# Kernel tuning notes

Measured on AMD Instinct MI355X. Metric: run time of the kernel, lower is better.

Reference implementation:

```python
import jax, jax.numpy as jnp
import numpy as np

HEADS = 12
D_MODEL = 768
D_K = D_MODEL // HEADS
BS, SEQ = 2, 4096


def setup_inputs() -> dict:
    key = jax.random.key(0)
    ks = jax.random.split(key, 12)
    s = 1.0 / np.sqrt(D_MODEL)
    return {
        "q": jax.random.normal(ks[0], (BS, SEQ, D_MODEL), jnp.float32),
        "k": jax.random.normal(ks[1], (BS, SEQ, D_MODEL), jnp.float32),
        "v": jax.random.normal(ks[2], (BS, SEQ, D_MODEL), jnp.float32),
        "Wq": jax.random.normal(ks[3], (D_MODEL, D_MODEL), jnp.float32) * s,
        "bq": jax.random.normal(ks[4], (D_MODEL,), jnp.float32) * s,
        "Wk": jax.random.normal(ks[5], (D_MODEL, D_MODEL), jnp.float32) * s,
        "bk": jax.random.normal(ks[6], (D_MODEL,), jnp.float32) * s,
        "Wv": jax.random.normal(ks[7], (D_MODEL, D_MODEL), jnp.float32) * s,
        "bv": jax.random.normal(ks[8], (D_MODEL,), jnp.float32) * s,
        "Wo": jax.random.normal(ks[9], (D_MODEL, D_MODEL), jnp.float32) * s,
        "bo": jax.random.normal(ks[10], (D_MODEL,), jnp.float32) * s,
        "mask": jnp.ones((BS, 1, SEQ), jnp.int32),
    }


def reference(q, k, v, Wq, bq, Wk, bk, Wv, bv, Wo, bo, mask):
    bs, sq, _ = q.shape
    # torch Linear: x @ W.T + b; then reshape to (bs, S, h, d_k) and transpose to (bs, h, S, d_k)
    def proj(x, W, b):
        y = x @ W.T + b
        return y.reshape(bs, -1, HEADS, D_K).transpose(0, 2, 1, 3)
    qh, kh, vh = proj(q, Wq, bq), proj(k, Wk, bk), proj(v, Wv, bv)
    scores = jnp.einsum("bhqd,bhkd->bhqk", qh, kh) / np.sqrt(D_K)
    # mask.unsqueeze(1): [bs,1,1,S_kv], masked_fill where mask == 0
    scores = jnp.where(mask[:, None, :, :] == 0, jnp.float32(-1e9), scores)
    attn = jax.nn.softmax(scores, axis=-1)  # dropout = identity (eval mode)
    ctx = jnp.einsum("bhqk,bhkd->bhqd", attn, vh)
    concat = ctx.transpose(0, 2, 1, 3).reshape(bs, sq, D_MODEL)
    return concat @ Wo.T + bo
```

## Files before the change

kernel.cpp:

```cpp
#include <hip/hip_runtime.h>
#include <hip/hip_bf16.h>

typedef __bf16 bf16x8 __attribute__((ext_vector_type(8)));
typedef __bf16 bf16x4 __attribute__((ext_vector_type(4)));
typedef short s16x4 __attribute__((ext_vector_type(4)));
typedef float f32x4 __attribute__((ext_vector_type(4)));
typedef unsigned short u16;

#define HEADS 12
#define DK 64
#define DM 768
#define SEQL 4096
#define BSZ 2
#define MROWS (BSZ * SEQL)
#define WELEM (DM * DM)
#define NX 6291456
#define WTOT (4 * WELEM)
#define BTOT (4 * 768)

#define QSCALE 0.180336880434245f
#define EXP2F(x) __builtin_amdgcn_exp2f(x)

__device__ __forceinline__ float bf2f(u16 x) {
    unsigned int u = ((unsigned int)x) << 16;
    return __uint_as_float(u);
}
__device__ __forceinline__ u16 f2bf(float f) {
    unsigned int u = __float_as_uint(f);
    u += 0x7fff + ((u >> 16) & 1);
    return (u16)(u >> 16);
}
__device__ __forceinline__ unsigned int cvt_pk(float lo, float hi) {
#if __has_builtin(__builtin_amdgcn_cvt_pk_bf16_f32)
    auto r = __builtin_amdgcn_cvt_pk_bf16_f32(lo, hi);
    unsigned int u;
    __builtin_memcpy(&u, &r, 4);
    return u;
#else
    return (unsigned int)f2bf(lo) | ((unsigned int)f2bf(hi) << 16);
#endif
}

__device__ __forceinline__ f32x4 mfma16(bf16x4 a, bf16x4 b, f32x4 c) {
#if __has_builtin(__builtin_amdgcn_mfma_f32_16x16x16_bf16)
    return __builtin_amdgcn_mfma_f32_16x16x16_bf16(a, b, c, 0, 0, 0);
#elif __has_builtin(__builtin_amdgcn_mfma_f32_16x16x16bf16_1k)
    s16x4 ai, bi;
    __builtin_memcpy(&ai, &a, 8);
    __builtin_memcpy(&bi, &b, 8);
    return __builtin_amdgcn_mfma_f32_16x16x16bf16_1k(ai, bi, c, 0, 0, 0);
#else
    f32x4 d = c;
    asm("v_mfma_f32_16x16x16_bf16 %0, %1, %2, %0" : "+v"(d) : "v"(a), "v"(b));
    return d;
#endif
}

__global__ void detect_dtype(const u16* __restrict__ q, int* __restrict__ flag) {
    __shared__ int cnt;
    if (threadIdx.x == 0) cnt = 0;
    __syncthreads();
    int c = 0;
    for (int i = threadIdx.x; i < 16384; i += 256) {
        u16 x = q[i];
        if (((x >> 7) & 0xFF) == 0xFF) c++;
    }
    if (c) atomicAdd(&cnt, c);
    __syncthreads();
    if (threadIdx.x == 0) *flag = (cnt > 0) ? 1 : 0;
}

__global__ __launch_bounds__(256) void convert_x(
    const void* __restrict__ X0, const void* __restrict__ X1, const void* __restrict__ X2,
    u16* __restrict__ Xc, const int* __restrict__ flag) {
    const int f32m = *flag;
    int i8 = blockIdx.x * 256 + threadIdx.x;
    if (i8 >= 3 * NX / 8) return;
    int w = i8 / (NX / 8);
    int off8 = i8 - w * (NX / 8);
    const void* src = (w == 0) ? X0 : (w == 1) ? X1 : X2;
    u16* dst = Xc + (size_t)w * NX + (size_t)off8 * 8;
    if (f32m) {
        float4 f0 = ((const float4*)src)[off8 * 2];
        float4 f1 = ((const float4*)src)[off8 * 2 + 1];
        uint4 p = {cvt_pk(f0.x, f0.y), cvt_pk(f0.z, f0.w),
                   cvt_pk(f1.x, f1.y), cvt_pk(f1.z, f1.w)};
        *(uint4*)dst = p;
    } else {
        *(uint4*)dst = ((const uint4*)src)[off8];
    }
}

__global__ __launch_bounds__(256) void convert_wb(
    const void* __restrict__ W0, const void* __restrict__ W1,
    const void* __restrict__ W2, const void* __restrict__ W3,
    const void* __restrict__ B0, const void* __restrict__ B1,
    const void* __restrict__ B2, const void* __restrict__ B3,
    u16* __restrict__ Wc, u16* __restrict__ bc, const int* __restrict__ flag) {
    const int f32m = *flag;
    int i4 = blockIdx.x * 256 + threadIdx.x;
    const int n4 = (WTOT + BTOT) / 4;
    if (i4 >= n4) return;
    int base = i4 * 4;
    const void* src;
    u16* dst;
    int off;
    if (base < WTOT) {
        int w = base / WELEM;
        off = base - w * WELEM;
        src = (w == 0) ? W0 : (w == 1) ? W1 : (w == 2) ? W2 : W3;
        dst = Wc + w * WELEM + off;
    } else {
        int bi = base - WTOT;
        int w = bi / 768;
        off = bi - w * 768;
        src = (w == 0) ? B0 : (w == 1) ? B1 : (w == 2) ? B2 : B3;
        dst = bc + w * 768 + off;
    }
    if (f32m) {
        float4 f = *(const float4*)((const float*)src + off);
        uint2 p = {cvt_pk(f.x, f.y), cvt_pk(f.z, f.w)};
        *(uint2*)dst = p;
    } else {
        *(uint2*)dst = *(const uint2*)((const u16*)src + off);
    }
}

typedef __attribute__((address_space(1))) unsigned int glb_u32;
typedef __attribute__((address_space(3))) unsigned int lds_u32;

__device__ __forceinline__ void gld16(const u16* g, u16* l) {
    __builtin_amdgcn_global_load_lds((glb_u32*)g, (lds_u32*)l, 16, 0, 0);
}

template <int NCH>
__device__ __forceinline__ void stage_g(const u16* gbase, u16* lbase, int tid) {
#pragma unroll
    for (int it = 0; it < NCH / 256; ++it) {
        int c = it * 256 + tid;
        int row = c >> 2, p = c & 3;
        int gc = p ^ (row & 3);
        gld16(gbase + (size_t)row * DM + gc * 8, lbase + c * 8);
    }
}

__global__ __launch_bounds__(256) void gemm_qkv3(
    const u16* __restrict__ Xc, const u16* __restrict__ Wc, const u16* __restrict__ bc,
    u16* __restrict__ Yq, u16* __restrict__ Yk, u16* __restrict__ Yv) {
    __shared__ __align__(16) u16 As[2][128 * 32];
    __shared__ __align__(16) u16 Bs[2][128 * 32];

    const int by  = blockIdx.y;
    const int sel = by / 6;
    const int n0  = (by - sel * 6) * 128;
    const int m0  = blockIdx.x * 128;

    const u16* X  = Xc + (size_t)sel * NX;
    const u16* W  = Wc + (size_t)sel * WELEM;
    const u16* Bp = bc + sel * 768;
    u16* Y = sel == 0 ? Yq : (sel == 1 ? Yk : Yv);
    const float oscale = sel == 0 ? QSCALE : 1.0f;

    const int tid = threadIdx.x, lane = tid & 63, wave = tid >> 6;
    const int wr = (wave >> 1) * 64, wc2 = (wave & 1) * 64;
    const int l15 = lane & 15, quad = lane >> 4;
    const int ck = (quad ^ (l15 & 3)) * 8;

    f32x4 acc[4][4] = {};

    stage_g<512>(X + (size_t)m0 * DM, &As[0][0], tid);
    stage_g<512>(W + (size_t)n0 * DM, &Bs[0][0], tid);
    __syncthreads();

    for (int it = 0; it < 24; ++it) {
        const int cur = it & 1, nxt = cur ^ 1;
        if (it < 23) {
            stage_g<512>(X + (size_t)m0 * DM + (it + 1) * 32, &As[nxt][0], tid);
            stage_g<512>(W + (size_t)n0 * DM + (it + 1) * 32, &Bs[nxt][0], tid);
        }
        bf16x8 a[4], b[4];
#pragma unroll
        for (int i = 0; i < 4; ++i)
            a[i] = *(const bf16x8*)&As[cur][(wr + i * 16 + l15) * 32 + ck];
#pragma unroll
        for (int j = 0; j < 4; ++j)
            b[j] = *(const bf16x8*)&Bs[cur][(wc2 + j * 16 + l15) * 32 + ck];
#pragma unroll
        for (int i = 0; i < 4; ++i)
#pragma unroll
            for (int j = 0; j < 4; ++j)
                acc[i][j] = __builtin_amdgcn_mfma_f32_16x16x32_bf16(a[i], b[j], acc[i][j], 0, 0, 0);
        __syncthreads();
    }

#pragma unroll
    for (int j = 0; j < 4; ++j) {
        int o = n0 + wc2 + j * 16 + l15;
        float bv = bf2f(Bp[o]);
        int h = o >> 6, d = o & 63;
#pragma unroll
        for (int i = 0; i < 4; ++i) {
            int row0 = m0 + wr + i * 16 + quad * 4;
            int bb = row0 >> 12, s0 = row0 & (SEQL - 1);
            if (sel < 2) {
#pragma unroll
                for (int r = 0; r < 4; ++r)
                    Y[((bb * HEADS + h) << 18) + ((s0 + r) << 6) + d] =
                        f2bf((acc[i][j][r] + bv) * oscale);
            } else {
                uint2 p = {cvt_pk(acc[i][j][0] + bv, acc[i][j][1] + bv),
                           cvt_pk(acc[i][j][2] + bv, acc[i][j][3] + bv)};
                *(uint2*)&Y[((bb * HEADS + h) << 18) + (d << 12) + s0] = p;
            }
        }
    }
}

__global__ __launch_bounds__(256) void gemm_out3(const u16* __restrict__ X,
                                                 const u16* __restrict__ W,
                                                 const u16* __restrict__ Bp,
                                                 void* __restrict__ Y,
                                                 const int* __restrict__ flag) {
    __shared__ __align__(16) u16 As[2][64 * 32];
    __shared__ __align__(16) u16 Bs[2][128 * 32];

    const int f32mode = *flag;
    const int m0 = blockIdx.x * 64, n0 = blockIdx.y * 128;
    const int tid = threadIdx.x, lane = tid & 63, wave = tid >> 6;
    const int wr = (wave >> 1) * 32, wc2 = (wave & 1) * 64;
    const int l15 = lane & 15, quad = lane >> 4;
    const int ck = (quad ^ (l15 & 3)) * 8;

    f32x4 acc[2][4] = {};

    stage_g<256>(X + (size_t)m0 * DM, &As[0][0], tid);
    stage_g<512>(W + (size_t)n0 * DM, &Bs[0][0], tid);
    __syncthreads();

    for (int it = 0; it < 24; ++it) {
        const int cur = it & 1, nxt = cur ^ 1;
        if (it < 23) {
            stage_g<256>(X + (size_t)m0 * DM + (it + 1) * 32, &As[nxt][0], tid);
            stage_g<512>(W + (size_t)n0 * DM + (it + 1) * 32, &Bs[nxt][0], tid);
        }
        bf16x8 a[2], b[4];
#pragma unroll
        for (int i = 0; i < 2; ++i)
            a[i] = *(const bf16x8*)&As[cur][(wr + i * 16 + l15) * 32 + ck];
#pragma unroll
        for (int j = 0; j < 4; ++j)
            b[j] = *(const bf16x8*)&Bs[cur][(wc2 + j * 16 + l15) * 32 + ck];
#pragma unroll
        for (int i = 0; i < 2; ++i)
#pragma unroll
            for (int j = 0; j < 4; ++j)
                acc[i][j] = __builtin_amdgcn_mfma_f32_16x16x32_bf16(a[i], b[j], acc[i][j], 0, 0, 0);
        __syncthreads();
    }

#pragma unroll
    for (int j = 0; j < 4; ++j) {
        int o = n0 + wc2 + j * 16 + l15;
        float bv = bf2f(Bp[o]);
#pragma unroll
        for (int i = 0; i < 2; ++i)
#pragma unroll
            for (int r = 0; r < 4; ++r) {
                int row = m0 + wr + i * 16 + quad * 4 + r;
                float val = acc[i][j][r] + bv;
                if (f32mode) ((float*)Y)[(size_t)row * DM + o] = val;
                else         ((u16*)Y)[(size_t)row * DM + o] = f2bf(val);
            }
    }
}

__device__ __forceinline__ void stage8_bf16(u16* dst, const u16* src) {
    *(uint4*)dst = *(const uint4*)src;
}
__device__ __forceinline__ void stage16_bf16(u16* dst, const u16* src) {
    *(uint4*)dst = *(const uint4*)src;
    *(uint4*)(dst + 8) = *(const uint4*)(src + 8);
}
__device__ __forceinline__ void stage16_f32pk(u16* dst, const float* src) {
    float4 f0 = ((const float4*)src)[0];
    float4 f1 = ((const float4*)src)[1];
    float4 f2 = ((const float4*)src)[2];
    float4 f3 = ((const float4*)src)[3];
    uint4 lo = {cvt_pk(f0.x, f0.y), cvt_pk(f0.z, f0.w), cvt_pk(f1.x, f1.y), cvt_pk(f1.z, f1.w)};
    uint4 hi = {cvt_pk(f2.x, f2.y), cvt_pk(f2.z, f2.w), cvt_pk(f3.x, f3.y), cvt_pk(f3.z, f3.w)};
    *(uint4*)dst = lo;
    *(uint4*)(dst + 8) = hi;
}

__global__ __launch_bounds__(256) void gemm_qkv_fb(
    const void* __restrict__ Xq, const void* __restrict__ Xk, const void* __restrict__ Xv,
    const u16* __restrict__ Wc, const u16* __restrict__ bc,
    u16* __restrict__ Yq, u16* __restrict__ Yk, u16* __restrict__ Yv,
    const int* __restrict__ flag) {
    __shared__ __align__(16) u16 As[128][40];
    __shared__ __align__(16) u16 Bs[64][40];
    const int f32mode = *flag;
    const int by = blockIdx.y;
    const int sel = by / 12;
    const int n0 = (by - sel * 12) * 64;
    const int m0 = blockIdx.x * 128;
    const void* Xp = sel == 0 ? Xq : (sel == 1 ? Xk : Xv);
    const u16* Wp = Wc + sel * WELEM;
    const u16* Bp = bc + sel * 768;
    u16* Y = sel == 0 ? Yq : (sel == 1 ? Yk : Yv);
    const float oscale = sel == 0 ? QSCALE : 1.0f;
    const int tid = threadIdx.x, lane = tid & 63, wave = tid >> 6;
    const int wr = (wave >> 1) * 64, wc = (wave & 1) * 32;
    const int l15 = lane & 15, quad = lane >> 4;
    const int srA = tid >> 1, scA = (tid & 1) * 16;
    const int srB = tid >> 2, scB = (tid & 3) * 8;
    f32x4 acc[4][2] = {};
    const size_t xoff = (size_t)(m0 + srA) * DM + scA;
    const size_t woff = (size_t)(n0 + srB) * DM + scB;
    for (int kb = 0; kb < DM; kb += 32) {
        if (f32mode) stage16_f32pk(&As[srA][scA], (const float*)Xp + xoff + kb);
        else         stage16_bf16(&As[srA][scA], (const u16*)Xp + xoff + kb);
        stage8_bf16(&Bs[srB][scB], Wp + woff + kb);
        __syncthreads();
        bf16x8 a[4], b[2];
#pragma unroll
        for (int i = 0; i < 4; ++i) a[i] = *(const bf16x8*)&As[wr + i * 16 + l15][quad * 8];
#pragma unroll
        for (int j = 0; j < 2; ++j) b[j] = *(const bf16x8*)&Bs[wc + j * 16 + l15][quad * 8];
#pragma unroll
        for (int i = 0; i < 4; ++i)
#pragma unroll
            for (int j = 0; j < 2; ++j)
                acc[i][j] = __builtin_amdgcn_mfma_f32_16x16x32_bf16(a[i], b[j], acc[i][j], 0, 0, 0);
        __syncthreads();
    }
#pragma unroll
    for (int j = 0; j < 2; ++j) {
        int o = n0 + wc + j * 16 + l15;
        float bv = bf2f(Bp[o]);
#pragma unroll
        for (int i = 0; i < 4; ++i)
#pragma unroll
            for (int r = 0; r < 4; ++r) {
                int row = m0 + wr + i * 16 + quad * 4 + r;
                float val = (acc[i][j][r] + bv) * oscale;
                int bb = row >> 12, s = row & (SEQL - 1);
                int h = o >> 6, d = o & 63;
                if (sel < 2) Y[((bb * HEADS + h) << 18) + (s << 6) + d] = f2bf(val);
                else         Y[((bb * HEADS + h) << 18) + (d << 12) + s] = f2bf(val);
            }
    }
}

__global__ __launch_bounds__(256) void gemm_out_fb(const u16* __restrict__ X,
                                                   const u16* __restrict__ Wp,
                                                   const u16* __restrict__ Bp,
                                                   void* __restrict__ Y,
                                                   const int* __restrict__ flag) {
    __shared__ __align__(16) u16 As[128][40];
    __shared__ __align__(16) u16 Bs[64][40];
    const int f32mode = *flag;
    const int m0 = blockIdx.x * 128, n0 = blockIdx.y * 64;
    const int tid = threadIdx.x, lane = tid & 63, wave = tid >> 6;
    const int wr = (wave >> 1) * 64, wc = (wave & 1) * 32;
    const int l15 = lane & 15, quad = lane >> 4;
    const int srA = tid >> 1, scA = (tid & 1) * 16;
    const int srB = tid >> 2, scB = (tid & 3) * 8;
    f32x4 acc[4][2] = {};
    const size_t xoff = (size_t)(m0 + srA) * DM + scA;
    const size_t woff = (size_t)(n0 + srB) * DM + scB;
    for (int kb = 0; kb < DM; kb += 32) {
        stage16_bf16(&As[srA][scA], X + xoff + kb);
        stage8_bf16(&Bs[srB][scB], Wp + woff + kb);
        __syncthreads();
        bf16x8 a[4], b[2];
#pragma unroll
        for (int i = 0; i < 4; ++i) a[i] = *(const bf16x8*)&As[wr + i * 16 + l15][quad * 8];
#pragma unroll
        for (int j = 0; j < 2; ++j) b[j] = *(const bf16x8*)&Bs[wc + j * 16 + l15][quad * 8];
#pragma unroll
        for (int i = 0; i < 4; ++i)
#pragma unroll
            for (int j = 0; j < 2; ++j)
                acc[i][j] = __builtin_amdgcn_mfma_f32_16x16x32_bf16(a[i], b[j], acc[i][j], 0, 0, 0);
        __syncthreads();
    }
#pragma unroll
    for (int j = 0; j < 2; ++j) {
        int o = n0 + wc + j * 16 + l15;
        float bv = bf2f(Bp[o]);
#pragma unroll
        for (int i = 0; i < 4; ++i)
#pragma unroll
            for (int r = 0; r < 4; ++r) {
                int row = m0 + wr + i * 16 + quad * 4 + r;
                float val = acc[i][j][r] + bv;
                if (f32mode) ((float*)Y)[(size_t)row * DM + o] = val;
                else         ((u16*)Y)[(size_t)row * DM + o] = f2bf(val);
            }
    }
}

__device__ __forceinline__ void stage_tile(const u16* gbase, int rstride,
                                           u16* lbase, int tid) {
#pragma unroll
    for (int it = 0; it < 2; ++it) {
        int c = it * 256 + tid;
        int row = c >> 3, p = c & 7;
        int gc = p ^ (row & 7);
        gld16(gbase + (size_t)row * rstride + gc * 8, lbase + c * 8);
    }
}

__global__ __launch_bounds__(256, 3) void flash_attn(const u16* __restrict__ Q,
                                                     const u16* __restrict__ K,
                                                     const u16* __restrict__ Vt,
                                                     const int* __restrict__ mask,
                                                     u16* __restrict__ ctx) {
    __shared__ __align__(16) u16 KVs[2][2][64 * 64];
    __shared__ __align__(16) float Ms[2][64];
    __shared__ int Mf[2];

    const int tid  = threadIdx.x;
    const int lane = tid & 63;
    const int wave = tid >> 6;
    const int l15  = lane & 15;
    const int quad = lane >> 4;

    const int bh = blockIdx.y;
    const int b  = bh / HEADS;
    const int h  = bh - b * HEADS;
    const int qb = blockIdx.x * 128 + wave * 32;

    const u16* Qh = Q  + ((size_t)bh << 18);
    const u16* Kh = K  + ((size_t)bh << 18);
    const u16* Vh = Vt + ((size_t)bh << 18);
    const int* maskb = mask + b * SEQL;

    bf16x8 aq[2][2];
#pragma unroll
    for (int s = 0; s < 2; ++s)
#pragma unroll
        for (int c = 0; c < 2; ++c)
            aq[s][c] = *(const bf16x8*)&Qh[(size_t)(qb + s * 16 + l15) * DK + c * 32 + quad * 8];

    const int r7   = l15 & 7;
    const int ck0  = (quad ^ r7) * 8;
    const int ck1  = ((quad + 4) ^ r7) * 8;
    const int lrow = l15 * 64;
    const int vq   = quad >> 1;
    const int voff = (quad & 1) * 4;

    float m_s[2] = {-3.0e38f, -3.0e38f}, l_s[2] = {0.f, 0.f};
    f32x4 o_acc[2][4] = {};

    int mreg = 0;
    if (tid < 64) mreg = maskb[tid];
    stage_tile(Kh, DK, &KVs[0][0][0], tid);
    stage_tile(Vh, SEQL, &KVs[0][1][0], tid);
    if (tid < 64) {
        int anym = __any(mreg == 0);
        Ms[0][tid] = (mreg == 0) ? -1.0e9f : 0.0f;
        if (tid == 0) Mf[0] = anym;
        mreg = maskb[64 + tid];
    }
    __syncthreads();

    for (int t = 0; t < 64; ++t) {
        const int cur = t & 1, nxt = cur ^ 1;
        if (t < 63) {
            const int kt = (t + 1) * 64;
            stage_tile(Kh + (size_t)kt * DK, DK, &KVs[nxt][0][0], tid);
            stage_tile(Vh + kt, SEQL, &KVs[nxt][1][0], tid);
            if (tid < 64) {
                int anym = __any(mreg == 0);
                Ms[nxt][tid] = (mreg == 0) ? -1.0e9f : 0.0f;
                if (tid == 0) Mf[nxt] = anym;
                if (t < 62) mreg = maskb[(t + 2) * 64 + tid];
            }
        }

        const u16* kb = &KVs[cur][0][0];
        const u16* vb = &KVs[cur][1][0];
        const int usebias = Mf[cur];

        f32x4 s4[2][4];
#pragma unroll
        for (int nt = 0; nt < 4; ++nt) {
            bf16x8 ak0 = *(const bf16x8*)&kb[lrow + nt * 1024 + ck0];
            bf16x8 ak1 = *(const bf16x8*)&kb[lrow + nt * 1024 + ck1];
#pragma unroll
            for (int s = 0; s < 2; ++s) {
                f32x4 z = {};
                z = __builtin_amdgcn_mfma_f32_16x16x32_bf16(ak0, aq[s][0], z, 0, 0, 0);
                z = __builtin_amdgcn_mfma_f32_16x16x32_bf16(ak1, aq[s][1], z, 0, 0, 0);
                s4[s][nt] = z;
            }
        }
        if (usebias) {
#pragma unroll
            for (int nt = 0; nt < 4; ++nt) {
                f32x4 bias = *(const f32x4*)&Ms[cur][nt * 16 + quad * 4];
#pragma unroll
                for (int s = 0; s < 2; ++s)
#pragma unroll
                    for (int r = 0; r < 4; ++r) s4[s][nt][r] += bias[r];
            }
        }

        float newm[2], rs[2];
#pragma unroll
        for (int s = 0; s < 2; ++s) {
            float t0 = fmaxf(fmaxf(s4[s][0][0], s4[s][0][1]), fmaxf(s4[s][0][2], s4[s][0][3]));
            float t1 = fmaxf(fmaxf(s4[s][1][0], s4[s][1][1]), fmaxf(s4[s][1][2], s4[s][1][3]));
            float t2 = fmaxf(fmaxf(s4[s][2][0], s4[s][2][1]), fmaxf(s4[s][2][2], s4[s][2][3]));
            float t3 = fmaxf(fmaxf(s4[s][3][0], s4[s][3][1]), fmaxf(s4[s][3][2], s4[s][3][3]));
            float mx = fmaxf(fmaxf(t0, t1), fmaxf(t2, t3));
            mx = fmaxf(mx, __shfl_xor(mx, 16, 64));
            mx = fmaxf(mx, __shfl_xor(mx, 32, 64));
            newm[s] = fmaxf(m_s[s], mx);

            f32x4 psum = {};
#pragma unroll
            for (int nt = 0; nt < 4; ++nt)
#pragma unroll
                for (int r = 0; r < 4; ++r) {
                    float p = EXP2F(s4[s][nt][r] - newm[s]);
                    s4[s][nt][r] = p;
                    psum[nt] += p;
                }
            float r2 = (psum[0] + psum[1]) + (psum[2] + psum[3]);
            r2 += __shfl_xor(r2, 16, 64);
            r2 += __shfl_xor(r2, 32, 64);
            rs[s] = r2;
        }

        if (!__all(newm[0] == m_s[0] && newm[1] == m_s[1])) {
#pragma unroll
            for (int s = 0; s < 2; ++s) {
                float alpha = EXP2F(m_s[s] - newm[s]);
                l_s[s] *= alpha;
#pragma unroll
                for (int dv = 0; dv < 4; ++dv)
#pragma unroll
                    for (int r = 0; r < 4; ++r) o_acc[s][dv][r] *= alpha;
                m_s[s] = newm[s];
            }
        }
        l_s[0] += rs[0];
        l_s[1] += rs[1];

        bf16x4 pp[2][4];
#pragma unroll
        for (int s = 0; s < 2; ++s)
#pragma unroll
            for (int nt = 0; nt < 4; ++nt) {
                uint2 cv = {cvt_pk(s4[s][nt][0], s4[s][nt][1]),
                            cvt_pk(s4[s][nt][2], s4[s][nt][3])};
                __builtin_memcpy(&pp[s][nt], &cv, 8);
            }

        bf16x4 av[4][4];
#pragma unroll
        for (int dv = 0; dv < 4; ++dv)
#pragma unroll
            for (int nt = 0; nt < 4; ++nt)
                av[dv][nt] = *(const bf16x4*)&vb[(dv * 16 + l15) * 64 +
                                                (((nt << 1) | vq) ^ r7) * 8 + voff];

        __builtin_amdgcn_s_setprio(1);
#pragma unroll
        for (int nt = 0; nt < 4; ++nt)
#pragma unroll
            for (int dv = 0; dv < 4; ++dv)
#pragma unroll
                for (int s = 0; s < 2; ++s)
                    o_acc[s][dv] = mfma16(av[dv][nt], pp[s][nt], o_acc[s][dv]);
        __builtin_amdgcn_s_setprio(0);
        __syncthreads();
    }

    u16* eb = &KVs[0][0][0] + wave * 2304;
#pragma unroll
    for (int s = 0; s < 2; ++s) {
        float inv = 1.0f / l_s[s];
#pragma unroll
        for (int dv = 0; dv < 4; ++dv) {
            uint2 cv = {cvt_pk(o_acc[s][dv][0] * inv, o_acc[s][dv][1] * inv),
                        cvt_pk(o_acc[s][dv][2] * inv, o_acc[s][dv][3] * inv)};
            *(uint2*)&eb[(s * 16 + l15) * 72 + dv * 16 + quad * 4] = cv;
        }
    }
    asm volatile("" ::: "memory");
    {
        int rowq = lane >> 2, dchunk = lane & 3;
#pragma unroll
        for (int s = 0; s < 2; ++s) {
            uint4 w0 = *(const uint4*)&eb[(s * 16 + rowq) * 72 + dchunk * 16];
            uint4 w1 = *(const uint4*)&eb[(s * 16 + rowq) * 72 + dchunk * 16 + 8];
            size_t orow = (size_t)(b * SEQL + qb + s * 16 + rowq) * DM + h * DK + dchunk * 16;
            *(uint4*)&ctx[orow] = w0;
            *(uint4*)&ctx[orow + 8] = w1;
        }
    }
}

extern "C" void kernel_launch(void* const* d_in, const int* in_sizes, int n_in,
                              void* d_out, int out_size, void* d_ws, size_t ws_size,
                              hipStream_t stream) {
    const void* q   = d_in[0];
    const void* k   = d_in[1];
    const void* v   = d_in[2];
    const void* Wq  = d_in[3];
    const void* bq  = d_in[4];
    const void* Wk  = d_in[5];
    const void* bk  = d_in[6];
    const void* Wv  = d_in[7];
    const void* bv  = d_in[8];
    const void* Wo  = d_in[9];
    const void* bo  = d_in[10];
    const int* mask = (const int*)d_in[11];

    const size_t NSH = (size_t)NX;
    u16* ws = (u16*)d_ws;

    const size_t need_full = (6 * NSH + WTOT + BTOT) * sizeof(u16) + 64;
    const size_t need_fb   = (4 * NSH + WTOT + BTOT) * sizeof(u16) + 64;

    if (ws_size >= need_full) {
        u16* Qh  = ws;
        u16* Kh  = ws + NSH;
        u16* Vth = ws + 2 * NSH;
        u16* Xc  = ws + 3 * NSH;
        u16* ctx = Xc;
        u16* Wc  = ws + 6 * NSH;
        u16* bc  = Wc + WTOT;
        int* dflag = (int*)(bc + BTOT);

        detect_dtype<<<1, 256, 0, stream>>>((const u16*)q, dflag);
        convert_x<<<(3 * NX / 8 + 255) / 256, 256, 0, stream>>>(q, k, v, Xc, dflag);
        convert_wb<<<((WTOT + BTOT) / 4 + 255) / 256, 256, 0, stream>>>(
            Wq, Wk, Wv, Wo, bq, bk, bv, bo, Wc, bc, dflag);

        gemm_qkv3<<<dim3(MROWS / 128, 18), 256, 0, stream>>>(Xc, Wc, bc, Qh, Kh, Vth);
        flash_attn<<<dim3(SEQL / 128, BSZ * HEADS), 256, 0, stream>>>(Qh, Kh, Vth, mask, ctx);
        gemm_out3<<<dim3(MROWS / 64, 6), 256, 0, stream>>>(
            ctx, Wc + 3 * (size_t)WELEM, bc + 3 * 768, d_out, dflag);
    } else if (ws_size >= need_fb) {
        u16* Qh  = ws;
        u16* Kh  = ws + NSH;
        u16* Vth = ws + 2 * NSH;
        u16* ctx = ws + 3 * NSH;
        u16* Wc  = ws + 4 * NSH;
        u16* bc  = Wc + WTOT;
        int* dflag = (int*)(bc + BTOT);

        detect_dtype<<<1, 256, 0, stream>>>((const u16*)q, dflag);
        convert_wb<<<((WTOT + BTOT) / 4 + 255) / 256, 256, 0, stream>>>(
            Wq, Wk, Wv, Wo, bq, bk, bv, bo, Wc, bc, dflag);
        gemm_qkv_fb<<<dim3(MROWS / 128, 36), 256, 0, stream>>>(
            q, k, v, Wc, bc, Qh, Kh, Vth, dflag);
        flash_attn<<<dim3(SEQL / 128, BSZ * HEADS), 256, 0, stream>>>(Qh, Kh, Vth, mask, ctx);
        gemm_out_fb<<<dim3(MROWS / 128, 12), 256, 0, stream>>>(
            ctx, Wc + 3 * (size_t)WELEM, bc + 3 * 768, d_out, dflag);
    }
}
```

Measured before the change: 403.1 us.

## Use 16x16x32 MFMA for PV, defer row-sum reduction, skip mask work when unmasked

The PV product now runs on 16x16x32 bf16 MFMAs instead of 16x16x16, halving the MFMA instruction count. To do this, P fragments are packed into bf16x8 and V fragments are built from two 8-byte LDS reads. The per-tile cross-lane shuffle reduction of the softmax row sum is moved to a single reduction at the end. A block-wide prescan of the whole mask row skips per-tile mask staging and bias add when no entry is zero. The prescan adds 16 global loads per thread and two barriers. The loop is also unrolled by 2 and the max reduction tree is reshaped.

```diff
diff --git a/kernel.cpp b/kernel.cpp
--- a/kernel.cpp
+++ b/kernel.cpp
@@ -38,21 +38,6 @@
     return u;
 #else
     return (unsigned int)f2bf(lo) | ((unsigned int)f2bf(hi) << 16);
-#endif
-}
-
-__device__ __forceinline__ f32x4 mfma16(bf16x4 a, bf16x4 b, f32x4 c) {
-#if __has_builtin(__builtin_amdgcn_mfma_f32_16x16x16_bf16)
-    return __builtin_amdgcn_mfma_f32_16x16x16_bf16(a, b, c, 0, 0, 0);
-#elif __has_builtin(__builtin_amdgcn_mfma_f32_16x16x16bf16_1k)
-    s16x4 ai, bi;
-    __builtin_memcpy(&ai, &a, 8);
-    __builtin_memcpy(&bi, &b, 8);
-    return __builtin_amdgcn_mfma_f32_16x16x16bf16_1k(ai, bi, c, 0, 0, 0);
-#else
-    f32x4 d = c;
-    asm("v_mfma_f32_16x16x16_bf16 %0, %1, %2, %0" : "+v"(d) : "v"(a), "v"(b));
-    return d;
 #endif
 }
 
@@ -420,6 +405,7 @@
     __shared__ __align__(16) u16 KVs[2][2][64 * 64];
     __shared__ __align__(16) float Ms[2][64];
     __shared__ int Mf[2];
+    __shared__ int AnyM;
 
     const int tid  = threadIdx.x;
     const int lane = tid & 63;
@@ -437,12 +423,22 @@
     const u16* Vh = Vt + ((size_t)bh << 18);
     const int* maskb = mask + b * SEQL;
 
+    if (tid == 0) AnyM = 0;
+    int zf = 0;
+#pragma unroll
+    for (int i = 0; i < 16; ++i) zf |= (maskb[tid + i * 256] == 0);
+
     bf16x8 aq[2][2];
 #pragma unroll
     for (int s = 0; s < 2; ++s)
 #pragma unroll
         for (int c = 0; c < 2; ++c)
             aq[s][c] = *(const bf16x8*)&Qh[(size_t)(qb + s * 16 + l15) * DK + c * 32 + quad * 8];
+
+    __syncthreads();
+    if (zf) atomicOr(&AnyM, 1);
+    __syncthreads();
+    const int anym = AnyM;
 
     const int r7   = l15 & 7;
     const int ck0  = (quad ^ r7) * 8;
@@ -451,44 +447,45 @@
     const int vq   = quad >> 1;
     const int voff = (quad & 1) * 4;
 
-    float m_s[2] = {-3.0e38f, -3.0e38f}, l_s[2] = {0.f, 0.f};
+    float m_s[2] = {-3.0e38f, -3.0e38f};
+    float l_s[2] = {0.f, 0.f};
     f32x4 o_acc[2][4] = {};
 
-    int mreg = 0;
-    if (tid < 64) mreg = maskb[tid];
     stage_tile(Kh, DK, &KVs[0][0][0], tid);
     stage_tile(Vh, SEQL, &KVs[0][1][0], tid);
-    if (tid < 64) {
-        int anym = __any(mreg == 0);
+    int mreg = 0;
+    if (anym && tid < 64) {
+        mreg = maskb[tid];
+        int anyt = __any(mreg == 0);
         Ms[0][tid] = (mreg == 0) ? -1.0e9f : 0.0f;
-        if (tid == 0) Mf[0] = anym;
+        if (tid == 0) Mf[0] = anyt;
         mreg = maskb[64 + tid];
     }
     __syncthreads();
 
+#pragma unroll 2
     for (int t = 0; t < 64; ++t) {
         const int cur = t & 1, nxt = cur ^ 1;
         if (t < 63) {
             const int kt = (t + 1) * 64;
             stage_tile(Kh + (size_t)kt * DK, DK, &KVs[nxt][0][0], tid);
             stage_tile(Vh + kt, SEQL, &KVs[nxt][1][0], tid);
-            if (tid < 64) {
-                int anym = __any(mreg == 0);
+            if (anym && tid < 64) {
+                int anyt = __any(mreg == 0);
                 Ms[nxt][tid] = (mreg == 0) ? -1.0e9f : 0.0f;
-                if (tid == 0) Mf[nxt] = anym;
+                if (tid == 0) Mf[nxt] = anyt;
                 if (t < 62) mreg = maskb[(t + 2) * 64 + tid];
             }
         }
 
-        const u16* kb = &KVs[cur][0][0];
-        const u16* vb = &KVs[cur][1][0];
-        const int usebias = Mf[cur];
+        const u16* kb2 = &KVs[cur][0][0];
+        const u16* vb  = &KVs[cur][1][0];
 
         f32x4 s4[2][4];
 #pragma unroll
         for (int nt = 0; nt < 4; ++nt) {
-            bf16x8 ak0 = *(const bf16x8*)&kb[lrow + nt * 1024 + ck0];
-            bf16x8 ak1 = *(const bf16x8*)&kb[lrow + nt * 1024 + ck1];
+            bf16x8 ak0 = *(const bf16x8*)&kb2[lrow + nt * 1024 + ck0];
+            bf16x8 ak1 = *(const bf16x8*)&kb2[lrow + nt * 1024 + ck1];
 #pragma unroll
             for (int s = 0; s < 2; ++s) {
                 f32x4 z = {};
@@ -497,6 +494,7 @@
                 s4[s][nt] = z;
             }
         }
+        const int usebias = anym ? Mf[cur] : 0;
         if (usebias) {
 #pragma unroll
             for (int nt = 0; nt < 4; ++nt) {
@@ -508,31 +506,20 @@
             }
         }
 
-        float newm[2], rs[2];
+        float newm[2];
 #pragma unroll
         for (int s = 0; s < 2; ++s) {
-            float t0 = fmaxf(fmaxf(s4[s][0][0], s4[s][0][1]), fmaxf(s4[s][0][2], s4[s][0][3]));
-            float t1 = fmaxf(fmaxf(s4[s][1][0], s4[s][1][1]), fmaxf(s4[s][1][2], s4[s][1][3]));
-            float t2 = fmaxf(fmaxf(s4[s][2][0], s4[s][2][1]), fmaxf(s4[s][2][2], s4[s][2][3]));
-            float t3 = fmaxf(fmaxf(s4[s][3][0], s4[s][3][1]), fmaxf(s4[s][3][2], s4[s][3][3]));
-            float mx = fmaxf(fmaxf(t0, t1), fmaxf(t2, t3));
+            float a0 = fmaxf(fmaxf(s4[s][0][0], s4[s][0][1]), s4[s][0][2]);
+            float a1 = fmaxf(fmaxf(s4[s][0][3], s4[s][1][0]), s4[s][1][1]);
+            float a2 = fmaxf(fmaxf(s4[s][1][2], s4[s][1][3]), s4[s][2][0]);
+            float a3 = fmaxf(fmaxf(s4[s][2][1], s4[s][2][2]), s4[s][2][3]);
+            float a4 = fmaxf(fmaxf(s4[s][3][0], s4[s][3][1]), s4[s][3][2]);
+            float b0 = fmaxf(fmaxf(a0, a1), a2);
+            float b1 = fmaxf(fmaxf(a3, a4), s4[s][3][3]);
+            float mx = fmaxf(b0, b1);
             mx = fmaxf(mx, __shfl_xor(mx, 16, 64));
             mx = fmaxf(mx, __shfl_xor(mx, 32, 64));
             newm[s] = fmaxf(m_s[s], mx);
-
-            f32x4 psum = {};
-#pragma unroll
-            for (int nt = 0; nt < 4; ++nt)
-#pragma unroll
-                for (int r = 0; r < 4; ++r) {
-                    float p = EXP2F(s4[s][nt][r] - newm[s]);
-                    s4[s][nt][r] = p;
-                    psum[nt] += p;
-                }
-            float r2 = (psum[0] + psum[1]) + (psum[2] + psum[3]);
-            r2 += __shfl_xor(r2, 16, 64);
-            r2 += __shfl_xor(r2, 32, 64);
-            rs[s] = r2;
         }
 
         if (!__all(newm[0] == m_s[0] && newm[1] == m_s[1])) {
@@ -541,41 +528,59 @@
                 float alpha = EXP2F(m_s[s] - newm[s]);
                 l_s[s] *= alpha;
 #pragma unroll
-                for (int dv = 0; dv < 4; ++dv)
-#pragma unroll
-                    for (int r = 0; r < 4; ++r) o_acc[s][dv][r] *= alpha;
+                for (int dv = 0; dv < 4; ++dv) o_acc[s][dv] *= alpha;
                 m_s[s] = newm[s];
             }
         }
-        l_s[0] += rs[0];
-        l_s[1] += rs[1];
-
-        bf16x4 pp[2][4];
+
+#pragma unroll
+        for (int s = 0; s < 2; ++s) {
+            f32x4 ps = {};
+#pragma unroll
+            for (int nt = 0; nt < 4; ++nt) {
+                f32x4 e = s4[s][nt] - newm[s];
+                e[0] = EXP2F(e[0]); e[1] = EXP2F(e[1]);
+                e[2] = EXP2F(e[2]); e[3] = EXP2F(e[3]);
+                s4[s][nt] = e;
+                ps += e;
+            }
+            l_s[s] += (ps[0] + ps[1]) + (ps[2] + ps[3]);
+        }
+
+        bf16x8 pp[2][2];
 #pragma unroll
         for (int s = 0; s < 2; ++s)
 #pragma unroll
-            for (int nt = 0; nt < 4; ++nt) {
-                uint2 cv = {cvt_pk(s4[s][nt][0], s4[s][nt][1]),
-                            cvt_pk(s4[s][nt][2], s4[s][nt][3])};
-                __builtin_memcpy(&pp[s][nt], &cv, 8);
-            }
-
-        bf16x4 av[4][4];
-#pragma unroll
-        for (int dv = 0; dv < 4; ++dv)
-#pragma unroll
-            for (int nt = 0; nt < 4; ++nt)
-                av[dv][nt] = *(const bf16x4*)&vb[(dv * 16 + l15) * 64 +
-                                                (((nt << 1) | vq) ^ r7) * 8 + voff];
+            for (int kbi = 0; kbi < 2; ++kbi) {
+                uint4 cv = {cvt_pk(s4[s][2 * kbi][0],     s4[s][2 * kbi][1]),
+                            cvt_pk(s4[s][2 * kbi][2],     s4[s][2 * kbi][3]),
+                            cvt_pk(s4[s][2 * kbi + 1][0], s4[s][2 * kbi + 1][1]),
+                            cvt_pk(s4[s][2 * kbi + 1][2], s4[s][2 * kbi + 1][3])};
+                __builtin_memcpy(&pp[s][kbi], &cv, 16);
+            }
+
+        bf16x8 av[4][2];
+#pragma unroll
+        for (int dv = 0; dv < 4; ++dv) {
+            const u16* vr = &vb[(dv * 16 + l15) * 64];
+#pragma unroll
+            for (int kbi = 0; kbi < 2; ++kbi) {
+                uint2 lo = *(const uint2*)&vr[((kbi * 4 + vq) ^ r7) * 8 + voff];
+                uint2 hi = *(const uint2*)&vr[((kbi * 4 + 2 + vq) ^ r7) * 8 + voff];
+                uint4 cc = {lo.x, lo.y, hi.x, hi.y};
+                __builtin_memcpy(&av[dv][kbi], &cc, 16);
+            }
+        }
 
         __builtin_amdgcn_s_setprio(1);
 #pragma unroll
-        for (int nt = 0; nt < 4; ++nt)
+        for (int kbi = 0; kbi < 2; ++kbi)
 #pragma unroll
             for (int dv = 0; dv < 4; ++dv)
 #pragma unroll
                 for (int s = 0; s < 2; ++s)
-                    o_acc[s][dv] = mfma16(av[dv][nt], pp[s][nt], o_acc[s][dv]);
+                    o_acc[s][dv] = __builtin_amdgcn_mfma_f32_16x16x32_bf16(
+                        av[dv][kbi], pp[s][kbi], o_acc[s][dv], 0, 0, 0);
         __builtin_amdgcn_s_setprio(0);
         __syncthreads();
     }
@@ -583,7 +588,10 @@
     u16* eb = &KVs[0][0][0] + wave * 2304;
 #pragma unroll
     for (int s = 0; s < 2; ++s) {
-        float inv = 1.0f / l_s[s];
+        float lf = l_s[s];
+        lf += __shfl_xor(lf, 16, 64);
+        lf += __shfl_xor(lf, 32, 64);
+        float inv = 1.0f / lf;
 #pragma unroll
         for (int dv = 0; dv < 4; ++dv) {
             uint2 cv = {cvt_pk(o_acc[s][dv][0] * inv, o_acc[s][dv][1] * inv),
```

Result: faster. 392.6 us (-2.6%).
